# Kernel tuning notes

Measured on AMD Instinct MI355X. Metric: run time of the kernel, lower is better.

## Reference

```python
import jax, jax.numpy as jnp
import numpy as np

N_NODES = 50000


def spmm(rows, cols, vals, dense):
    # out[i,:] = sum_{e: rows[e]==i} vals[e] * dense[cols[e], :]
    gathered = dense[cols] * vals[:, None]  # [E, D]
    return jax.ops.segment_sum(gathered, rows, num_segments=N_NODES)


def setup_inputs() -> dict:
    key = jax.random.key(0)
    k1, k2, k3, k4, k5, k6 = jax.random.split(key, 6)
    N, E, F, H, C = N_NODES, 800000, 512, 256, 64
    node_features = jax.random.normal(k1, (N, F), dtype=jnp.float32)
    adj_rows = jax.random.randint(k2, (E,), 0, N, dtype=jnp.int32)
    adj_cols = jax.random.randint(k3, (E,), 0, N, dtype=jnp.int32)
    adj_vals = jax.random.uniform(k4, (E,), dtype=jnp.float32)
    W1 = jax.random.normal(k5, (F, H), dtype=jnp.float32) * (1.0 / np.sqrt(F))
    b1 = jnp.zeros((H,), dtype=jnp.float32)
    W2 = jax.random.normal(k6, (H, C), dtype=jnp.float32) * (1.0 / np.sqrt(H))
    b2 = jnp.zeros((C,), dtype=jnp.float32)
    return {"node_features": node_features, "adj_rows": adj_rows,
            "adj_cols": adj_cols, "adj_vals": adj_vals,
            "W1": W1, "b1": b1, "W2": W2, "b2": b2}


def reference(node_features, adj_rows, adj_cols, adj_vals, W1, b1, W2, b2):
    # Layer 1: dense projection then sparse aggregation, then ReLU.
    support1 = node_features @ W1 + b1           # [N, H]
    x = jax.nn.relu(spmm(adj_rows, adj_cols, adj_vals, support1))
    # Dropout is identity in eval mode (training=False).
    # Layer 2
    support2 = x @ W2 + b2                       # [N, C]
    x = spmm(adj_rows, adj_cols, adj_vals, support2)
    return jax.nn.log_softmax(x, axis=1)
```

## Files before the change

kernel.cpp:

```cpp
#include <hip/hip_runtime.h>

#define N_NODES 50000
#define N_EDGES 800000
#define F_IN    512
#define H_DIM   256
#define C_DIM   64
#define MPAD    50048

#define NB      196
#define NCHUNK  196
#define CHUNK   4096
#define BCAP    6144

typedef __bf16 bf16;
typedef __bf16 bf16x4 __attribute__((ext_vector_type(4)));
typedef __bf16 bf16x8 __attribute__((ext_vector_type(8)));
typedef float  f32x4  __attribute__((ext_vector_type(4)));
typedef unsigned int u32;
typedef unsigned long long u64;
typedef unsigned char u8;

__device__ __forceinline__ void gl_lds16(const void* g, void* l) {
    __builtin_amdgcn_global_load_lds(
        (const __attribute__((address_space(1))) u32*)g,
        (__attribute__((address_space(3))) u32*)l, 16, 0, 0);
}

__device__ __forceinline__ float unpack_val(u32 pk) {
    return __builtin_bit_cast(float, pk << 16);
}


__global__ __launch_bounds__(1024) void prep_k(const int* __restrict__ rows,
                                               const float* __restrict__ W1,
                                               const float* __restrict__ W2,
                                               u32* __restrict__ G,
                                               bf16* __restrict__ W1t,
                                               bf16* __restrict__ W2t) {
    __shared__ u32 h[16 * NB];
    int bid = blockIdx.x, tid = threadIdx.x;
    if (bid < NCHUNK) {
        int wid = tid >> 6;
        for (int i = tid; i < 16 * NB; i += 1024) h[i] = 0;
        __syncthreads();
        int base = bid * CHUNK;
        int end = base + CHUNK; if (end > N_EDGES) end = N_EDGES;
        for (int e = base + tid; e < end; e += 1024)
            atomicAdd(&h[wid * NB + (rows[e] >> 8)], 1);
        __syncthreads();
        if (tid < NB) {
            u32 s = 0;
#pragma unroll
            for (int w = 0; w < 16; w++) s += h[w * NB + tid];
            G[tid * NCHUNK + bid] = s;
        }
    } else {
        int i = (bid - NCHUNK) * 1024 + tid;
        if (i < F_IN * H_DIM) {
            int k = i >> 8, n = i & 255;
            W1t[n * F_IN + k] = (bf16)W1[i];
        } else {
            int j = i - F_IN * H_DIM;
            if (j < H_DIM * C_DIM) {
                int k = j >> 6, n = j & 63;
                W2t[n * H_DIM + k] = (bf16)W2[j];
            }
        }
    }
}


__global__ __launch_bounds__(512) void sg_k(const int* __restrict__ rows,
                                            const int* __restrict__ cols,
                                            const float* __restrict__ vals,
                                            const u32* __restrict__ G,
                                            u32* __restrict__ epckS,
                                            u8* __restrict__ lrowS,
                                            const float* __restrict__ A,
                                            const bf16* __restrict__ Bt,
                                            const float* __restrict__ bias,
                                            bf16* __restrict__ C) {
    __shared__ __attribute__((aligned(16))) char smem[40960];
    int bid = blockIdx.x, tid = threadIdx.x;
    int wid = tid >> 6, lane = tid & 63;

    if (bid < NCHUNK) {
        u32* sdat  = (u32*)smem;
        u8*  sbkt  = (u8*)(smem + 16384);
        u8*  srow  = (u8*)(smem + 20480);
        u32* h     = (u32*)(smem + 24576);
        u32* loff  = (u32*)(smem + 32768);
        u32* lcur  = (u32*)(smem + 33792);
        u32* gbase = (u32*)(smem + 34816);
        u32* wt    = (u32*)(smem + 35840);
        int c = bid;
        int base = c * CHUNK;
        int end = base + CHUNK; if (end > N_EDGES) end = N_EDGES;
        int n = end - base;

        for (int i = tid; i < 2048; i += 512) h[i] = 0;

        u32 tot = 0, pre = 0, incl = 0;
        if (tid < 256) {
            if (tid < NB) {
                for (int cc = 0; cc < NCHUNK; cc++) {
                    u32 v = G[tid * NCHUNK + cc];
                    tot += v;
                    if (cc < c) pre += v;
                }
            }
            incl = tot;
#pragma unroll
            for (int off = 1; off < 64; off <<= 1) {
                u32 u = __shfl_up(incl, off, 64);
                if (lane >= off) incl += u;
            }
            if (lane == 63) wt[wid] = incl;
        }
        __syncthreads();
        if (tid < 256) {
            u32 wpre = 0;
#pragma unroll
            for (int w = 0; w < 4; w++)
                if (w < wid) wpre += wt[w];
            if (tid < NB) gbase[tid] = (wpre + incl - tot) + pre;
        }

        u32 pk_r[8], b_r[8], lr_r[8];
#pragma unroll
        for (int j = 0; j < 8; j++) {
            int e = base + tid + j * 512;
            bool ok = e < end;
            int ee = ok ? e : base;
            int r = rows[ee];
            unsigned short vb = __builtin_bit_cast(unsigned short, (bf16)vals[ee]);
            pk_r[j] = ((u32)cols[ee] << 16) | (u32)vb;
            b_r[j] = (u32)(r >> 8);
            lr_r[j] = (u32)(r & 255);
            if (ok) atomicAdd(&h[wid * 256 + b_r[j]], 1);
        }
        __syncthreads();

        u32 t2 = 0, incl2 = 0;
        if (tid < 256) {
#pragma unroll
            for (int w2 = 0; w2 < 8; w2++) t2 += h[w2 * 256 + tid];
            incl2 = t2;
#pragma unroll
            for (int off = 1; off < 64; off <<= 1) {
                u32 u = __shfl_up(incl2, off, 64);
                if (lane >= off) incl2 += u;
            }
            if (lane == 63) wt[wid] = incl2;
        }
        __syncthreads();
        if (tid < 256) {
            u32 wpre2 = 0;
#pragma unroll
            for (int w = 0; w < 4; w++)
                if (w < wid) wpre2 += wt[w];
            u32 excl = wpre2 + incl2 - t2;
            loff[tid] = excl;
            lcur[tid] = excl;
        }
        __syncthreads();

#pragma unroll
        for (int j = 0; j < 8; j++) {
            int e = base + tid + j * 512;
            if (e < end) {
                u32 p = atomicAdd(&lcur[b_r[j]], 1);
                sdat[p] = pk_r[j];
                sbkt[p] = (u8)b_r[j];
                srow[p] = (u8)lr_r[j];
            }
        }
        __syncthreads();

        for (int i = tid; i < n; i += 512) {
            u32 b2 = sbkt[i];
            u32 dst = gbase[b2] + (u32)i - loff[b2];
            epckS[dst] = sdat[i];
            lrowS[dst] = srow[i];
        }
        return;
    }

    constexpr int BM = 64, BK = 64;
    bf16* As = (bf16*)smem;
    bf16* Bs = (bf16*)(smem + 8192);
    int l15 = lane & 15, hi = lane >> 4;
    int sw = l15 & 7;
    int bm = bid - NCHUNK;

    f32x4 acc[4][2];
#pragma unroll
    for (int m = 0; m < 4; m++)
#pragma unroll
        for (int n = 0; n < 2; n++) acc[m][n] = (f32x4){0.f, 0.f, 0.f, 0.f};

    for (int kt = 0; kt < F_IN; kt += BK) {
#pragma unroll
        for (int j = 0; j < 4; j++) {
            int ch = j * 512 + tid;
            int row = ch >> 3, kc = ch & 7;
            int kcs = kc ^ (row & 7);
            gl_lds16(Bt + (size_t)row * F_IN + kt + kcs * 8,
                     &Bs[(j * 512 + wid * 64) * 8]);
        }
        {
            int row = tid >> 3, kc = tid & 7;
            int ar = bm * BM + row;
            if (ar >= N_NODES) ar = N_NODES - 1;
            const f32x4* src = (const f32x4*)(A + (size_t)ar * F_IN + kt + kc * 8);
            f32x4 u = src[0], v = src[1];
            bf16x8 o;
            o[0] = (bf16)u[0]; o[1] = (bf16)u[1]; o[2] = (bf16)u[2]; o[3] = (bf16)u[3];
            o[4] = (bf16)v[0]; o[5] = (bf16)v[1]; o[6] = (bf16)v[2]; o[7] = (bf16)v[3];
            *(bf16x8*)&As[row * BK + (kc ^ (row & 7)) * 8] = o;
        }
        __syncthreads();

        bf16x8 afr[2][4], bfr[2][2];
#pragma unroll
        for (int kk = 0; kk < 2; kk++) {
            int c = (kk * 4 + hi) ^ sw;
#pragma unroll
            for (int m = 0; m < 4; m++)
                afr[kk][m] = *(const bf16x8*)&As[(m * 16 + l15) * BK + c * 8];
#pragma unroll
            for (int n = 0; n < 2; n++)
                bfr[kk][n] = *(const bf16x8*)&Bs[(wid * 32 + n * 16 + l15) * BK + c * 8];
        }
#pragma unroll
        for (int kk = 0; kk < 2; kk++)
#pragma unroll
            for (int m = 0; m < 4; m++)
#pragma unroll
                for (int n = 0; n < 2; n++)
                    acc[m][n] = __builtin_amdgcn_mfma_f32_16x16x32_bf16(
                        afr[kk][m], bfr[kk][n], acc[m][n], 0, 0, 0);
        __syncthreads();
    }

#pragma unroll
    for (int m = 0; m < 4; m++) {
        int row0 = bm * BM + m * 16 + hi * 4;
#pragma unroll
        for (int n = 0; n < 2; n++) {
            int col = wid * 32 + n * 16 + l15;
            float bz = bias[col];
#pragma unroll
            for (int r = 0; r < 4; r++) {
                int row = row0 + r;
                if (row < N_NODES)
                    C[(size_t)row * H_DIM + col] = (bf16)(acc[m][n][r] + bz);
            }
        }
    }
}


__global__ __launch_bounds__(256) void sortC_k(const u32* __restrict__ epckS,
                                               const u8* __restrict__ lrowS,
                                               const u32* __restrict__ G,
                                               u32* __restrict__ epack,
                                               int* __restrict__ starts) {
    __shared__ u32 edat[BCAP];
    __shared__ u32 sdat[BCAP];
    __shared__ u8  erow[BCAP];
    __shared__ u32 h[4 * 256];
    __shared__ u32 cur[256];
    __shared__ u32 wt1[4], wt2[4];
    __shared__ u32 sh_s, sh_n;
    int b = blockIdx.x, tid = threadIdx.x, wid = tid >> 6, lane = tid & 63;

    u32 btot = 0;
    if (tid < NB)
        for (int cc = 0; cc < NCHUNK; cc++) btot += G[tid * NCHUNK + cc];
    u32 bincl = btot;
#pragma unroll
    for (int off = 1; off < 64; off <<= 1) {
        u32 u = __shfl_up(bincl, off, 64);
        if (lane >= off) bincl += u;
    }
    if (lane == 63) wt1[wid] = bincl;
    __syncthreads();
    u32 bwpre = 0;
#pragma unroll
    for (int w = 0; w < 4; w++)
        if (w < wid) bwpre += wt1[w];
    if (tid == b) { sh_s = bwpre + bincl - btot; sh_n = btot; }
    __syncthreads();
    int s = (int)sh_s;
    int n = (int)sh_n;
    if (n > BCAP) n = BCAP;

    for (int i = tid; i < n; i += 256) { edat[i] = epckS[s + i]; erow[i] = lrowS[s + i]; }
    for (int i = tid; i < 1024; i += 256) h[i] = 0;
    __syncthreads();
    for (int i = tid; i < n; i += 256) atomicAdd(&h[wid * 256 + erow[i]], 1);
    __syncthreads();
    u32 tot = h[tid] + h[256 + tid] + h[512 + tid] + h[768 + tid];
    u32 incl = tot;
#pragma unroll
    for (int off = 1; off < 64; off <<= 1) {
        u32 u = __shfl_up(incl, off, 64);
        if (lane >= off) incl += u;
    }
    if (lane == 63) wt2[wid] = incl;
    __syncthreads();
    u32 wpre = 0;
#pragma unroll
    for (int w = 0; w < 4; w++)
        if (w < wid) wpre += wt2[w];
    u32 excl = wpre + incl - tot;
    cur[tid] = excl;
    int grow = b * 256 + tid;
    if (grow < N_NODES) starts[grow] = s + (int)excl;
    if (b == 0 && tid == 0) starts[N_NODES] = N_EDGES;
    __syncthreads();
    for (int i = tid; i < n; i += 256) {
        u32 p = atomicAdd(&cur[erow[i]], 1);
        sdat[p] = edat[i];
    }
    __syncthreads();
    for (int i = tid; i < n; i += 256) epack[s + i] = sdat[i];
}


__global__ __launch_bounds__(256) void gemm2_k(const bf16* __restrict__ A,
                                               const bf16* __restrict__ Bt,
                                               const float* __restrict__ bias,
                                               bf16* __restrict__ C) {
    constexpr int BM = 128, BK = 64;
    __shared__ bf16 As[BM * BK];
    __shared__ bf16 Bs[64 * BK];

    int tid = threadIdx.x;
    int wid = tid >> 6, lane = tid & 63;
    int wr = wid >> 1, wc = wid & 1;
    int l15 = lane & 15, hi = lane >> 4;
    int sw = l15 & 7;
    int bm = blockIdx.x;

    f32x4 acc[4][2];
#pragma unroll
    for (int m = 0; m < 4; m++)
#pragma unroll
        for (int n = 0; n < 2; n++) acc[m][n] = (f32x4){0.f, 0.f, 0.f, 0.f};

    for (int kt = 0; kt < H_DIM; kt += BK) {
#pragma unroll
        for (int j = 0; j < 4; j++) {
            int ch = j * 256 + tid;
            int row = ch >> 3, kc = ch & 7;
            int kcs = kc ^ (row & 7);
            gl_lds16(A + (size_t)(bm * BM + row) * H_DIM + kt + kcs * 8,
                     &As[(j * 256 + wid * 64) * 8]);
        }
#pragma unroll
        for (int j = 0; j < 2; j++) {
            int ch = j * 256 + tid;
            int row = ch >> 3, kc = ch & 7;
            int kcs = kc ^ (row & 7);
            gl_lds16(Bt + (size_t)row * H_DIM + kt + kcs * 8,
                     &Bs[(j * 256 + wid * 64) * 8]);
        }
        __syncthreads();

        bf16x8 afr[2][4], bfr[2][2];
#pragma unroll
        for (int kk = 0; kk < 2; kk++) {
            int c = (kk * 4 + hi) ^ sw;
#pragma unroll
            for (int m = 0; m < 4; m++)
                afr[kk][m] = *(const bf16x8*)&As[(wr * 64 + m * 16 + l15) * BK + c * 8];
#pragma unroll
            for (int n = 0; n < 2; n++)
                bfr[kk][n] = *(const bf16x8*)&Bs[(wc * 32 + n * 16 + l15) * BK + c * 8];
        }
#pragma unroll
        for (int kk = 0; kk < 2; kk++)
#pragma unroll
            for (int m = 0; m < 4; m++)
#pragma unroll
                for (int n = 0; n < 2; n++)
                    acc[m][n] = __builtin_amdgcn_mfma_f32_16x16x32_bf16(
                        afr[kk][m], bfr[kk][n], acc[m][n], 0, 0, 0);
        __syncthreads();
    }

#pragma unroll
    for (int m = 0; m < 4; m++) {
        int row0 = bm * BM + wr * 64 + m * 16 + hi * 4;
#pragma unroll
        for (int n = 0; n < 2; n++) {
            int col = wc * 32 + n * 16 + l15;
            float bz = bias[col];
#pragma unroll
            for (int r = 0; r < 4; r++) {
                int row = row0 + r;
                if (row < N_NODES)
                    C[(size_t)row * C_DIM + col] = (bf16)(acc[m][n][r] + bz);
            }
        }
    }
}


__global__ __launch_bounds__(256) void spmm1_k(const int* __restrict__ starts,
                                               const u32* __restrict__ epack,
                                               const bf16* __restrict__ s1,
                                               bf16* __restrict__ x16) {
    int wid = threadIdx.x >> 6, lane = threadIdx.x & 63;
    int row = blockIdx.x * 4 + wid;
    if (row >= N_NODES) return;
    int s = starts[row], e = starts[row + 1];
    f32x4 acc = (f32x4){0.f, 0.f, 0.f, 0.f};
    const bf16* s1l = s1 + lane * 4;
    int p = s;
    for (; p + 8 <= e; p += 8) {
        u32 k0 = __builtin_nontemporal_load(epack + p);
        u32 k1 = __builtin_nontemporal_load(epack + p + 1);
        u32 k2 = __builtin_nontemporal_load(epack + p + 2);
        u32 k3 = __builtin_nontemporal_load(epack + p + 3);
        u32 k4 = __builtin_nontemporal_load(epack + p + 4);
        u32 k5 = __builtin_nontemporal_load(epack + p + 5);
        u32 k6 = __builtin_nontemporal_load(epack + p + 6);
        u32 k7 = __builtin_nontemporal_load(epack + p + 7);
        bf16x4 g0 = *(const bf16x4*)(s1l + (size_t)(k0 >> 16) * H_DIM);
        bf16x4 g1 = *(const bf16x4*)(s1l + (size_t)(k1 >> 16) * H_DIM);
        bf16x4 g2 = *(const bf16x4*)(s1l + (size_t)(k2 >> 16) * H_DIM);
        bf16x4 g3 = *(const bf16x4*)(s1l + (size_t)(k3 >> 16) * H_DIM);
        bf16x4 g4 = *(const bf16x4*)(s1l + (size_t)(k4 >> 16) * H_DIM);
        bf16x4 g5 = *(const bf16x4*)(s1l + (size_t)(k5 >> 16) * H_DIM);
        bf16x4 g6 = *(const bf16x4*)(s1l + (size_t)(k6 >> 16) * H_DIM);
        bf16x4 g7 = *(const bf16x4*)(s1l + (size_t)(k7 >> 16) * H_DIM);
        float v0 = unpack_val(k0), v1 = unpack_val(k1), v2 = unpack_val(k2), v3 = unpack_val(k3);
        float v4 = unpack_val(k4), v5 = unpack_val(k5), v6 = unpack_val(k6), v7 = unpack_val(k7);
#pragma unroll
        for (int j = 0; j < 4; j++)
            acc[j] += v0 * (float)g0[j] + v1 * (float)g1[j] +
                      v2 * (float)g2[j] + v3 * (float)g3[j] +
                      v4 * (float)g4[j] + v5 * (float)g5[j] +
                      v6 * (float)g6[j] + v7 * (float)g7[j];
    }
    for (; p < e; ++p) {
        u32 k = __builtin_nontemporal_load(epack + p);
        float v = unpack_val(k);
        bf16x4 g = *(const bf16x4*)(s1l + (size_t)(k >> 16) * H_DIM);
#pragma unroll
        for (int j = 0; j < 4; j++) acc[j] += v * (float)g[j];
    }
    bf16x4 o;
#pragma unroll
    for (int j = 0; j < 4; j++) o[j] = (bf16)fmaxf(acc[j], 0.f);
    u64 bits = __builtin_bit_cast(u64, o);
    __builtin_nontemporal_store(bits, (u64*)(x16 + (size_t)row * H_DIM + lane * 4));
}


__global__ __launch_bounds__(256) void spmm2_sm_k(const int* __restrict__ starts,
                                                  const u32* __restrict__ epack,
                                                  const bf16* __restrict__ s2,
                                                  float* __restrict__ out) {
    int wid = threadIdx.x >> 6, lane = threadIdx.x & 63;
    int row = blockIdx.x * 4 + wid;
    if (row >= N_NODES) return;
    int s = starts[row], e = starts[row + 1];
    float acc = 0.f;
    int p = s;
    for (; p + 8 <= e; p += 8) {
        u32 k0 = __builtin_nontemporal_load(epack + p);
        u32 k1 = __builtin_nontemporal_load(epack + p + 1);
        u32 k2 = __builtin_nontemporal_load(epack + p + 2);
        u32 k3 = __builtin_nontemporal_load(epack + p + 3);
        u32 k4 = __builtin_nontemporal_load(epack + p + 4);
        u32 k5 = __builtin_nontemporal_load(epack + p + 5);
        u32 k6 = __builtin_nontemporal_load(epack + p + 6);
        u32 k7 = __builtin_nontemporal_load(epack + p + 7);
        float g0 = (float)s2[(size_t)(k0 >> 16) * C_DIM + lane];
        float g1 = (float)s2[(size_t)(k1 >> 16) * C_DIM + lane];
        float g2 = (float)s2[(size_t)(k2 >> 16) * C_DIM + lane];
        float g3 = (float)s2[(size_t)(k3 >> 16) * C_DIM + lane];
        float g4 = (float)s2[(size_t)(k4 >> 16) * C_DIM + lane];
        float g5 = (float)s2[(size_t)(k5 >> 16) * C_DIM + lane];
        float g6 = (float)s2[(size_t)(k6 >> 16) * C_DIM + lane];
        float g7 = (float)s2[(size_t)(k7 >> 16) * C_DIM + lane];
        acc += unpack_val(k0) * g0 + unpack_val(k1) * g1 +
               unpack_val(k2) * g2 + unpack_val(k3) * g3 +
               unpack_val(k4) * g4 + unpack_val(k5) * g5 +
               unpack_val(k6) * g6 + unpack_val(k7) * g7;
    }
    for (; p < e; ++p) {
        u32 k = __builtin_nontemporal_load(epack + p);
        acc += unpack_val(k) * (float)s2[(size_t)(k >> 16) * C_DIM + lane];
    }
    float mx = acc;
#pragma unroll
    for (int off = 32; off >= 1; off >>= 1) mx = fmaxf(mx, __shfl_xor(mx, off, 64));
    float ex = expf(acc - mx);
    float se = ex;
#pragma unroll
    for (int off = 32; off >= 1; off >>= 1) se += __shfl_xor(se, off, 64);
    __builtin_nontemporal_store((acc - mx) - logf(se),
                                out + (size_t)row * C_DIM + lane);
}


extern "C" void kernel_launch(void* const* d_in, const int* in_sizes, int n_in,
                              void* d_out, int out_size, void* d_ws, size_t ws_size,
                              hipStream_t stream) {
    const float* nf   = (const float*)d_in[0];
    const int*   rows = (const int*)d_in[1];
    const int*   cols = (const int*)d_in[2];
    const float* vals = (const float*)d_in[3];
    const float* W1   = (const float*)d_in[4];
    const float* b1   = (const float*)d_in[5];
    const float* W2   = (const float*)d_in[6];
    const float* b2   = (const float*)d_in[7];
    float* out = (float*)d_out;

    char* w = (char*)d_ws;
    auto alloc = [&](size_t b) { void* p = (void*)w; w += (b + 255) & ~(size_t)255; return p; };

    bf16* x16  = (bf16*)alloc((size_t)MPAD * H_DIM * 2);
    bf16* sup1 = (bf16*)alloc((size_t)N_NODES * H_DIM * 2);
    bf16* sup2 = sup1;
    bf16* W1t = (bf16*)alloc((size_t)H_DIM * F_IN * 2);
    bf16* W2t = (bf16*)alloc((size_t)C_DIM * H_DIM * 2);
    int* starts = (int*)alloc((size_t)(N_NODES + 1) * 4);
    u32* G      = (u32*)alloc((size_t)NB * NCHUNK * 4);
    u32* epack  = (u32*)alloc((size_t)N_EDGES * 4);
    u32* epckS  = (u32*)alloc((size_t)N_EDGES * 4);
    u8*  lrowS  = (u8*)alloc((size_t)N_EDGES);

    prep_k<<<NCHUNK + 144, 1024, 0, stream>>>(rows, W1, W2, G, W1t, W2t);
    sg_k<<<NCHUNK + MPAD / 64, 512, 0, stream>>>(rows, cols, vals, G, epckS, lrowS,
                                                 nf, W1t, b1, sup1);
    sortC_k<<<NB, 256, 0, stream>>>(epckS, lrowS, G, epack, starts);
    spmm1_k<<<(N_NODES + 3) / 4, 256, 0, stream>>>(starts, epack, sup1, x16);
    gemm2_k<<<MPAD / 128, 256, 0, stream>>>(x16, W2t, b2, sup2);
    spmm2_sm_k<<<(N_NODES + 3) / 4, 256, 0, stream>>>(starts, epack, sup2, out);

    (void)in_sizes; (void)n_in; (void)out_size; (void)ws_size;
}
```

Baseline: 166.2 us.

## Move GEMM1 co-scheduling from scatter kernel to bucket-sort kernel

The chunk scatter pass is split into its own 1024-thread kernel. GEMM1 now shares a launch with the per-bucket counting sort instead of the scatter, so the sort work overlaps the dense projection. The sort blocks now use 512 threads and stream epckS directly rather than staging it in LDS first. This changes which phase hides behind the GEMM and gives the sort more threads, while the scatter no longer overlaps with anything.

```diff
diff --git a/kernel.cpp b/kernel.cpp
--- a/kernel.cpp
+++ b/kernel.cpp
@@ -70,119 +70,199 @@
 }
 
 
-__global__ __launch_bounds__(512) void sg_k(const int* __restrict__ rows,
-                                            const int* __restrict__ cols,
-                                            const float* __restrict__ vals,
-                                            const u32* __restrict__ G,
-                                            u32* __restrict__ epckS,
-                                            u8* __restrict__ lrowS,
-                                            const float* __restrict__ A,
-                                            const bf16* __restrict__ Bt,
-                                            const float* __restrict__ bias,
-                                            bf16* __restrict__ C) {
+__global__ __launch_bounds__(1024) void scat_k(const int* __restrict__ rows,
+                                               const int* __restrict__ cols,
+                                               const float* __restrict__ vals,
+                                               const u32* __restrict__ G,
+                                               u32* __restrict__ epckS,
+                                               u8* __restrict__ lrowS) {
+    __shared__ u32 sdat[CHUNK];
+    __shared__ u8  sbkt[CHUNK];
+    __shared__ u8  srow[CHUNK];
+    __shared__ u32 h[16 * 256];
+    __shared__ u32 loff[256], lcur[256], gbase[256];
+    __shared__ u32 wt[16];
+    int tid = threadIdx.x, wid = tid >> 6, lane = tid & 63;
+    int c = blockIdx.x;
+    int base = c * CHUNK;
+    int end = base + CHUNK; if (end > N_EDGES) end = N_EDGES;
+    int n = end - base;
+
+    for (int i = tid; i < 4096; i += 1024) h[i] = 0;
+
+    u32 tot = 0, pre = 0, incl = 0;
+    if (tid < 256) {
+        if (tid < NB) {
+            for (int cc = 0; cc < NCHUNK; cc++) {
+                u32 v = G[tid * NCHUNK + cc];
+                tot += v;
+                if (cc < c) pre += v;
+            }
+        }
+        incl = tot;
+#pragma unroll
+        for (int off = 1; off < 64; off <<= 1) {
+            u32 u = __shfl_up(incl, off, 64);
+            if (lane >= off) incl += u;
+        }
+        if (lane == 63) wt[wid] = incl;
+    }
+    __syncthreads();
+    if (tid < 256) {
+        u32 wpre = 0;
+#pragma unroll
+        for (int w = 0; w < 4; w++)
+            if (w < wid) wpre += wt[w];
+        if (tid < NB) gbase[tid] = (wpre + incl - tot) + pre;
+    }
+
+    u32 pk_r[4], b_r[4], lr_r[4];
+#pragma unroll
+    for (int j = 0; j < 4; j++) {
+        int e = base + tid + j * 1024;
+        bool ok = e < end;
+        int ee = ok ? e : base;
+        int r = rows[ee];
+        unsigned short vb = __builtin_bit_cast(unsigned short, (bf16)vals[ee]);
+        pk_r[j] = ((u32)cols[ee] << 16) | (u32)vb;
+        b_r[j] = (u32)(r >> 8);
+        lr_r[j] = (u32)(r & 255);
+        if (ok) atomicAdd(&h[wid * 256 + b_r[j]], 1);
+    }
+    __syncthreads();
+
+    u32 t2 = 0, incl2 = 0;
+    if (tid < 256) {
+#pragma unroll
+        for (int w2 = 0; w2 < 16; w2++) t2 += h[w2 * 256 + tid];
+        incl2 = t2;
+#pragma unroll
+        for (int off = 1; off < 64; off <<= 1) {
+            u32 u = __shfl_up(incl2, off, 64);
+            if (lane >= off) incl2 += u;
+        }
+        if (lane == 63) wt[wid] = incl2;
+    }
+    __syncthreads();
+    if (tid < 256) {
+        u32 wpre2 = 0;
+#pragma unroll
+        for (int w = 0; w < 4; w++)
+            if (w < wid) wpre2 += wt[w];
+        u32 excl = wpre2 + incl2 - t2;
+        loff[tid] = excl;
+        lcur[tid] = excl;
+    }
+    __syncthreads();
+
+#pragma unroll
+    for (int j = 0; j < 4; j++) {
+        int e = base + tid + j * 1024;
+        if (e < end) {
+            u32 p = atomicAdd(&lcur[b_r[j]], 1);
+            sdat[p] = pk_r[j];
+            sbkt[p] = (u8)b_r[j];
+            srow[p] = (u8)lr_r[j];
+        }
+    }
+    __syncthreads();
+
+    for (int i = tid; i < n; i += 1024) {
+        u32 b2 = sbkt[i];
+        u32 dst = gbase[b2] + (u32)i - loff[b2];
+        epckS[dst] = sdat[i];
+        lrowS[dst] = srow[i];
+    }
+}
+
+
+__global__ __launch_bounds__(512) void sg2_k(const u32* __restrict__ epckS,
+                                             const u8* __restrict__ lrowS,
+                                             const u32* __restrict__ G,
+                                             u32* __restrict__ epack,
+                                             int* __restrict__ starts,
+                                             const float* __restrict__ A,
+                                             const bf16* __restrict__ Bt,
+                                             const float* __restrict__ bias,
+                                             bf16* __restrict__ C) {
     __shared__ __attribute__((aligned(16))) char smem[40960];
     int bid = blockIdx.x, tid = threadIdx.x;
     int wid = tid >> 6, lane = tid & 63;
 
-    if (bid < NCHUNK) {
-        u32* sdat  = (u32*)smem;
-        u8*  sbkt  = (u8*)(smem + 16384);
-        u8*  srow  = (u8*)(smem + 20480);
-        u32* h     = (u32*)(smem + 24576);
-        u32* loff  = (u32*)(smem + 32768);
-        u32* lcur  = (u32*)(smem + 33792);
-        u32* gbase = (u32*)(smem + 34816);
-        u32* wt    = (u32*)(smem + 35840);
-        int c = bid;
-        int base = c * CHUNK;
-        int end = base + CHUNK; if (end > N_EDGES) end = N_EDGES;
-        int n = end - base;
+    if (bid < NB) {
+        u32* sdat = (u32*)smem;
+        u8*  erow = (u8*)(smem + 24576);
+        u32* h    = (u32*)(smem + 30720);
+        u32* cur  = (u32*)(smem + 38912);
+        u32* wt1  = (u32*)(smem + 39936);
+        u32* shsn = (u32*)(smem + 39952);
+        int b = bid;
+
+        u32 btot = 0, bincl = 0;
+        if (tid < 256) {
+            if (tid < NB)
+                for (int cc = 0; cc < NCHUNK; cc++) btot += G[tid * NCHUNK + cc];
+            bincl = btot;
+#pragma unroll
+            for (int off = 1; off < 64; off <<= 1) {
+                u32 u = __shfl_up(bincl, off, 64);
+                if (lane >= off) bincl += u;
+            }
+            if (lane == 63) wt1[wid] = bincl;
+        }
+        __syncthreads();
+        if (tid < 256) {
+            u32 bwpre = 0;
+#pragma unroll
+            for (int w = 0; w < 4; w++)
+                if (w < wid) bwpre += wt1[w];
+            if (tid == b) { shsn[0] = bwpre + bincl - btot; shsn[1] = btot; }
+        }
+        __syncthreads();
+        int s = (int)shsn[0];
+        int n = (int)shsn[1];
+        if (n > BCAP) n = BCAP;
 
         for (int i = tid; i < 2048; i += 512) h[i] = 0;
-
-        u32 tot = 0, pre = 0, incl = 0;
+        __syncthreads();
+        for (int i = tid; i < n; i += 512) {
+            u8 r = lrowS[s + i];
+            erow[i] = r;
+            atomicAdd(&h[wid * 256 + r], 1);
+        }
+        __syncthreads();
+        u32 tot = 0, incl = 0;
         if (tid < 256) {
-            if (tid < NB) {
-                for (int cc = 0; cc < NCHUNK; cc++) {
-                    u32 v = G[tid * NCHUNK + cc];
-                    tot += v;
-                    if (cc < c) pre += v;
-                }
-            }
+#pragma unroll
+            for (int w = 0; w < 8; w++) tot += h[w * 256 + tid];
             incl = tot;
 #pragma unroll
             for (int off = 1; off < 64; off <<= 1) {
                 u32 u = __shfl_up(incl, off, 64);
                 if (lane >= off) incl += u;
             }
-            if (lane == 63) wt[wid] = incl;
+            if (lane == 63) wt1[wid] = incl;
         }
         __syncthreads();
         if (tid < 256) {
             u32 wpre = 0;
 #pragma unroll
             for (int w = 0; w < 4; w++)
-                if (w < wid) wpre += wt[w];
-            if (tid < NB) gbase[tid] = (wpre + incl - tot) + pre;
-        }
-
-        u32 pk_r[8], b_r[8], lr_r[8];
-#pragma unroll
-        for (int j = 0; j < 8; j++) {
-            int e = base + tid + j * 512;
-            bool ok = e < end;
-            int ee = ok ? e : base;
-            int r = rows[ee];
-            unsigned short vb = __builtin_bit_cast(unsigned short, (bf16)vals[ee]);
-            pk_r[j] = ((u32)cols[ee] << 16) | (u32)vb;
-            b_r[j] = (u32)(r >> 8);
-            lr_r[j] = (u32)(r & 255);
-            if (ok) atomicAdd(&h[wid * 256 + b_r[j]], 1);
-        }
-        __syncthreads();
-
-        u32 t2 = 0, incl2 = 0;
-        if (tid < 256) {
-#pragma unroll
-            for (int w2 = 0; w2 < 8; w2++) t2 += h[w2 * 256 + tid];
-            incl2 = t2;
-#pragma unroll
-            for (int off = 1; off < 64; off <<= 1) {
-                u32 u = __shfl_up(incl2, off, 64);
-                if (lane >= off) incl2 += u;
-            }
-            if (lane == 63) wt[wid] = incl2;
-        }
-        __syncthreads();
-        if (tid < 256) {
-            u32 wpre2 = 0;
-#pragma unroll
-            for (int w = 0; w < 4; w++)
-                if (w < wid) wpre2 += wt[w];
-            u32 excl = wpre2 + incl2 - t2;
-            loff[tid] = excl;
-            lcur[tid] = excl;
-        }
-        __syncthreads();
-
-#pragma unroll
-        for (int j = 0; j < 8; j++) {
-            int e = base + tid + j * 512;
-            if (e < end) {
-                u32 p = atomicAdd(&lcur[b_r[j]], 1);
-                sdat[p] = pk_r[j];
-                sbkt[p] = (u8)b_r[j];
-                srow[p] = (u8)lr_r[j];
-            }
-        }
-        __syncthreads();
-
+                if (w < wid) wpre += wt1[w];
+            u32 excl = wpre + incl - tot;
+            cur[tid] = excl;
+            int grow = b * 256 + tid;
+            if (grow < N_NODES) starts[grow] = s + (int)excl;
+        }
+        if (b == 0 && tid == 0) starts[N_NODES] = N_EDGES;
+        __syncthreads();
         for (int i = tid; i < n; i += 512) {
-            u32 b2 = sbkt[i];
-            u32 dst = gbase[b2] + (u32)i - loff[b2];
-            epckS[dst] = sdat[i];
-            lrowS[dst] = srow[i];
-        }
+            u32 v = epckS[s + i];
+            u32 p = atomicAdd(&cur[erow[i]], 1);
+            sdat[p] = v;
+        }
+        __syncthreads();
+        for (int i = tid; i < n; i += 512) epack[s + i] = sdat[i];
         return;
     }
 
@@ -191,7 +271,7 @@
     bf16* Bs = (bf16*)(smem + 8192);
     int l15 = lane & 15, hi = lane >> 4;
     int sw = l15 & 7;
-    int bm = bid - NCHUNK;
+    int bm = bid - NB;
 
     f32x4 acc[4][2];
 #pragma unroll
@@ -258,74 +338,6 @@
             }
         }
     }
-}
-
-
-__global__ __launch_bounds__(256) void sortC_k(const u32* __restrict__ epckS,
-                                               const u8* __restrict__ lrowS,
-                                               const u32* __restrict__ G,
-                                               u32* __restrict__ epack,
-                                               int* __restrict__ starts) {
-    __shared__ u32 edat[BCAP];
-    __shared__ u32 sdat[BCAP];
-    __shared__ u8  erow[BCAP];
-    __shared__ u32 h[4 * 256];
-    __shared__ u32 cur[256];
-    __shared__ u32 wt1[4], wt2[4];
-    __shared__ u32 sh_s, sh_n;
-    int b = blockIdx.x, tid = threadIdx.x, wid = tid >> 6, lane = tid & 63;
-
-    u32 btot = 0;
-    if (tid < NB)
-        for (int cc = 0; cc < NCHUNK; cc++) btot += G[tid * NCHUNK + cc];
-    u32 bincl = btot;
-#pragma unroll
-    for (int off = 1; off < 64; off <<= 1) {
-        u32 u = __shfl_up(bincl, off, 64);
-        if (lane >= off) bincl += u;
-    }
-    if (lane == 63) wt1[wid] = bincl;
-    __syncthreads();
-    u32 bwpre = 0;
-#pragma unroll
-    for (int w = 0; w < 4; w++)
-        if (w < wid) bwpre += wt1[w];
-    if (tid == b) { sh_s = bwpre + bincl - btot; sh_n = btot; }
-    __syncthreads();
-    int s = (int)sh_s;
-    int n = (int)sh_n;
-    if (n > BCAP) n = BCAP;
-
-    for (int i = tid; i < n; i += 256) { edat[i] = epckS[s + i]; erow[i] = lrowS[s + i]; }
-    for (int i = tid; i < 1024; i += 256) h[i] = 0;
-    __syncthreads();
-    for (int i = tid; i < n; i += 256) atomicAdd(&h[wid * 256 + erow[i]], 1);
-    __syncthreads();
-    u32 tot = h[tid] + h[256 + tid] + h[512 + tid] + h[768 + tid];
-    u32 incl = tot;
-#pragma unroll
-    for (int off = 1; off < 64; off <<= 1) {
-        u32 u = __shfl_up(incl, off, 64);
-        if (lane >= off) incl += u;
-    }
-    if (lane == 63) wt2[wid] = incl;
-    __syncthreads();
-    u32 wpre = 0;
-#pragma unroll
-    for (int w = 0; w < 4; w++)
-        if (w < wid) wpre += wt2[w];
-    u32 excl = wpre + incl - tot;
-    cur[tid] = excl;
-    int grow = b * 256 + tid;
-    if (grow < N_NODES) starts[grow] = s + (int)excl;
-    if (b == 0 && tid == 0) starts[N_NODES] = N_EDGES;
-    __syncthreads();
-    for (int i = tid; i < n; i += 256) {
-        u32 p = atomicAdd(&cur[erow[i]], 1);
-        sdat[p] = edat[i];
-    }
-    __syncthreads();
-    for (int i = tid; i < n; i += 256) epack[s + i] = sdat[i];
 }
 
 
@@ -537,9 +549,9 @@
     u8*  lrowS  = (u8*)alloc((size_t)N_EDGES);
 
     prep_k<<<NCHUNK + 144, 1024, 0, stream>>>(rows, W1, W2, G, W1t, W2t);
-    sg_k<<<NCHUNK + MPAD / 64, 512, 0, stream>>>(rows, cols, vals, G, epckS, lrowS,
-                                                 nf, W1t, b1, sup1);
-    sortC_k<<<NB, 256, 0, stream>>>(epckS, lrowS, G, epack, starts);
+    scat_k<<<NCHUNK, 1024, 0, stream>>>(rows, cols, vals, G, epckS, lrowS);
+    sg2_k<<<NB + MPAD / 64, 512, 0, stream>>>(epckS, lrowS, G, epack, starts,
+                                              nf, W1t, b1, sup1);
     spmm1_k<<<(N_NODES + 3) / 4, 256, 0, stream>>>(starts, epack, sup1, x16);
     gemm2_k<<<MPAD / 128, 256, 0, stream>>>(x16, W2t, b2, sup2);
     spmm2_sm_k<<<(N_NODES + 3) / 4, 256, 0, stream>>>(starts, epack, sup2, out);
```

Measured after the change: 164.1 us. No clear change (-1.3%).
